# Optimization experiments

Hardware: AMD Instinct MI355X
Metric: run time of the kernel (lower is better)

## Reference

```python
import jax, jax.numpy as jnp
import numpy as np

# dimensions
N = 50000    # nodes
E = 600000   # edges
NS = 64      # scalar (0e) channels of node features
NV = 32      # vector (1o) channels of node features
A = 16       # node attr channels (16x0e)
R = 8        # edge embedding dim (radial basis, 8x0e)
H = 8        # fc_hidden_size
AVG_NB = 12.0  # avg_num_neighbors
# gate layout: NS scalars (silu) + NV gate scalars (sigmoid) gating NV vectors
GS = NS + NV  # 96 scalar channels before gate
NW = NS + NS + NV + NV  # 192 per-edge TP weights (paths: s*Y0->0e, s*Y1->1o, v*Y0->1o, v.Y1->0e)


def setup_inputs() -> dict:
    key = jax.random.key(0)
    ks = jax.random.split(key, 20)
    d = {
        'node_s': jax.random.normal(ks[0], (N, NS), jnp.float32),
        'node_v': jax.random.normal(ks[1], (N, NV, 3), jnp.float32),
        'node_attrs': jax.random.normal(ks[2], (N, A), jnp.float32),
        'edge_emb': jax.random.uniform(ks[3], (E, R), jnp.float32),
        'edge_sh0': jnp.ones((E, 1), jnp.float32),
        'edge_sh1': jax.random.normal(ks[4], (E, 3), jnp.float32),
        'edge_index': jax.random.randint(ks[5], (2, E), 0, N),
        # linear_1 on node feats (per-irrep channel mixing)
        'W1s': jax.random.normal(ks[6], (NS, NS), jnp.float32),
        'W1v': jax.random.normal(ks[7], (NV, NV), jnp.float32),
        # radial MLP producing per-edge TP weights
        'Wm1': jax.random.normal(ks[8], (R, H), jnp.float32),
        'Wm2': jax.random.normal(ks[9], (H, NW), jnp.float32),
        # linear_2: TP out (96x0e+96x1o) -> pre-gate (96x0e+32x1o)
        'W2s': jax.random.normal(ks[10], (GS, GS), jnp.float32),
        'W2v': jax.random.normal(ks[11], (NS + NV, NV), jnp.float32),
        # update UVU TP internal weights (msg x attrs)
        'Wt0': jax.random.normal(ks[12], (NS, A), jnp.float32),
        'Wt1': jax.random.normal(ks[13], (NV, A), jnp.float32),
        # linear_3
        'W3s': jax.random.normal(ks[14], (NS, GS), jnp.float32),
        'W3v': jax.random.normal(ks[15], (NV, NV), jnp.float32),
        # self connection: FullyConnectedTensorProduct(node_feats, attrs -> pre-gate)
        'Wsc0': jax.random.normal(ks[16], (NS, A, GS), jnp.float32),
        'Wsc1': jax.random.normal(ks[17], (NV, A, NV), jnp.float32),
    }
    return d


def _gate(s_all, v):
    # s_all: [.., GS]; first NS scalars -> silu, last NV -> sigmoid gates for vectors
    scal = jax.nn.silu(s_all[..., :NS])
    gates = jax.nn.sigmoid(s_all[..., NS:])
    return scal, v * gates[..., None]


def reference(node_s, node_v, node_attrs, edge_emb, edge_sh0, edge_sh1, edge_index,
              W1s, W1v, Wm1, Wm2, W2s, W2v, Wt0, Wt1, W3s, W3v, Wsc0, Wsc1):
    src, dst = edge_index[0], edge_index[1]

    # ---- message ----
    s1 = (node_s @ W1s) / jnp.sqrt(jnp.float32(NS))                       # [N,NS]
    v1 = jnp.einsum('nuc,uv->nvc', node_v, W1v) / jnp.sqrt(jnp.float32(NV))
    ss = s1[src]   # [E,NS]
    vv = v1[src]   # [E,NV,3]

    # per-edge TP weights from radial MLP
    w = jax.nn.silu(edge_emb @ Wm1) @ Wm2                                 # [E,NW]
    w0a, w1a, w1b, w0b = jnp.split(w, [NS, 2 * NS, 2 * NS + NV], axis=1)

    # UVU tensor product with SH edge attrs (lmax=1)
    t0a = w0a * ss * edge_sh0                                             # [E,NS] 0e
    t0b = w0b * jnp.einsum('euc,ec->eu', vv, edge_sh1)                    # [E,NV] 0e
    t1a = w1a[:, :, None] * ss[:, :, None] * edge_sh1[:, None, :]         # [E,NS,3] 1o
    t1b = w1b[:, :, None] * vv * edge_sh0[:, :, None]                     # [E,NV,3] 1o
    tp_s = jnp.concatenate([t0a, t0b], axis=1)                            # [E,96]
    tp_v = jnp.concatenate([t1a, t1b], axis=1)                            # [E,96,3]

    m_s = (tp_s @ W2s) / jnp.sqrt(jnp.float32(GS))                        # [E,GS]
    m_v = jnp.einsum('euc,uv->evc', tp_v, W2v) / jnp.sqrt(jnp.float32(NS + NV))  # [E,NV,3]
    msg_s, msg_v = _gate(m_s, m_v)                                        # [E,NS], [E,NV,3]

    # ---- update ----
    agg_s = jax.ops.segment_sum(msg_s, dst, num_segments=N) / jnp.sqrt(jnp.float32(AVG_NB))
    agg_v = jax.ops.segment_sum(msg_v, dst, num_segments=N) / jnp.sqrt(jnp.float32(AVG_NB))

    u0 = jnp.einsum('nu,na,ua->nu', agg_s, node_attrs, Wt0) / jnp.sqrt(jnp.float32(A))
    u1 = jnp.einsum('nuc,na,ua->nuc', agg_v, node_attrs, Wt1) / jnp.sqrt(jnp.float32(A))

    f_s = (u0 @ W3s) / jnp.sqrt(jnp.float32(NS))                          # [N,GS]
    f_v = jnp.einsum('nuc,uv->nvc', u1, W3v) / jnp.sqrt(jnp.float32(NV))  # [N,NV,3]

    # self connection (fully connected TP with scalar attrs)
    sc_s = jnp.einsum('nu,na,uav->nv', node_s, node_attrs, Wsc0) / jnp.sqrt(jnp.float32(NS * A))
    sc_v = jnp.einsum('nuc,na,uaw->nwc', node_v, node_attrs, Wsc1) / jnp.sqrt(jnp.float32(NV * A))
    f_s = f_s + sc_s
    f_v = f_v + sc_v

    out_s, out_v = _gate(f_s, f_v)                                        # [N,NS], [N,NV,3]
    return jnp.concatenate([out_s, out_v.reshape(N, NV * 3)], axis=1)     # [N,160]
```

## Files before the change

kernel.cpp:

```cpp
#include <hip/hip_runtime.h>
#include <math.h>

#define N 50000
#define E 600000
#define EPB 16
#define LDK 104

typedef __attribute__((ext_vector_type(8))) short short8;
typedef __attribute__((ext_vector_type(4))) float float4v;

__device__ __forceinline__ float silu_f(float x) { return x / (1.f + __expf(-x)); }
__device__ __forceinline__ float sigm_f(float x) { return 1.f / (1.f + __expf(-x)); }
__device__ __forceinline__ unsigned short f2bf(float f) {
  unsigned u = __float_as_uint(f);
  u += 0x7fff + ((u >> 16) & 1);
  return (unsigned short)(u >> 16);
}
__device__ __forceinline__ float bf2f(unsigned short u) {
  return __uint_as_float(((unsigned)u) << 16);
}

__global__ void k_hist(const int* __restrict__ eidx, int* __restrict__ counts) {
  int e = blockIdx.x * 256 + threadIdx.x;
  if (e < E) atomicAdd(&counts[eidx[E + e]], 1);
}

__global__ __launch_bounds__(1024)
void k_scan(const int* __restrict__ counts, int* __restrict__ row_ptr) {
  __shared__ int ssum[1024];
  const int t = threadIdx.x;
  const int CH = 49;
  int lo = t * CH, hi = min(lo + CH, N);
  int s = 0;
  for (int i = lo; i < hi; i++) s += counts[i];
  ssum[t] = s;
  __syncthreads();
  for (int off = 1; off < 1024; off <<= 1) {
    int v = (t >= off) ? ssum[t - off] : 0;
    __syncthreads();
    ssum[t] += v;
    __syncthreads();
  }
  int run = (t == 0) ? 0 : ssum[t - 1];
  for (int i = lo; i < hi; i++) { row_ptr[i] = run; run += counts[i]; }
  if (t == 1023) row_ptr[N] = ssum[1023];
}

__global__ void k_scatter(const int* __restrict__ eidx, const int* __restrict__ row_ptr,
                          int* __restrict__ woff, int* __restrict__ perm) {
  int e = blockIdx.x * 256 + threadIdx.x;
  if (e < E) {
    int d = eidx[E + e];
    int p = atomicAdd(&woff[d], 1);
    perm[row_ptr[d] + p] = e;
  }
}

__global__ void k_prep(const float* __restrict__ Wsc0, const float* __restrict__ W3s,
                       const float* __restrict__ Wsc1, const float* __restrict__ W3v,
                       const float* __restrict__ W2s, const float* __restrict__ W2v,
                       unsigned short* __restrict__ BT, unsigned short* __restrict__ B2T,
                       unsigned short* __restrict__ w2sTg, unsigned short* __restrict__ w2vTg) {
  const float isq96 = 0.10206207261596575f;
  int i = blockIdx.x * 256 + threadIdx.x;
  if (i < 96 * 1088) {
    int j = i / 1088, k = i % 1088;
    float v;
    if (k < 1024) v = Wsc0[(size_t)k * 96 + j] * 0.03125f;
    else          v = W3s[(size_t)(k - 1024) * 96 + j] * 0.125f;
    BT[i] = f2bf(v);
  } else if (i < 96 * 1088 + 32 * 576) {
    int i2 = i - 96 * 1088;
    int w = i2 / 576, k = i2 % 576;
    float v = 0.f;
    if (k < 512)      v = Wsc1[(size_t)k * 32 + w] * 0.04419417382415922f;
    else if (k < 544) v = W3v[(size_t)(k - 512) * 32 + w] * 0.17677669529663689f;
    B2T[i2] = f2bf(v);
  } else if (i < 96 * 1088 + 32 * 576 + 96 * 96) {
    int i3 = i - (96 * 1088 + 32 * 576);
    int j = i3 / 96, k = i3 % 96;
    w2sTg[i3] = f2bf(W2s[(size_t)k * 96 + j] * isq96);
  } else {
    int i4 = i - (96 * 1088 + 32 * 576 + 96 * 96);
    if (i4 < 32 * 96) {
      int v = i4 / 96, u = i4 % 96;
      w2vTg[i4] = f2bf(W2v[(size_t)u * 32 + v] * isq96);
    }
  }
}

__global__ __launch_bounds__(256, 4)
void k_lin1(const float* __restrict__ node_s, const float* __restrict__ node_v,
            const float* __restrict__ W1s, const float* __restrict__ W1v,
            float* __restrict__ s1, float* __restrict__ v1) {
  __shared__ float w1s[64 * 64];
  __shared__ float w1v[32 * 32];
  for (int i = threadIdx.x; i < 64 * 64; i += 256) w1s[i] = W1s[i];
  for (int i = threadIdx.x; i < 32 * 32; i += 256) w1v[i] = W1v[i];
  __syncthreads();
  const float is_ns = 0.125f;
  const float is_nv = 0.17677669529663689f;
  int gtid = blockIdx.x * 256 + threadIdx.x;
  int stride = gridDim.x * 256;
  for (int i = gtid; i < N * 160; i += stride) {
    int n = i / 160, ch = i % 160;
    if (ch < 64) {
      const float* row = node_s + n * 64;
      float acc = 0.f;
#pragma unroll
      for (int u = 0; u < 64; u++) acc += row[u] * w1s[u * 64 + ch];
      s1[n * 64 + ch] = acc * is_ns;
    } else {
      int p = ch - 64, v = p / 3, c = p % 3;
      const float* row = node_v + n * 96;
      float acc = 0.f;
#pragma unroll
      for (int u = 0; u < 32; u++) acc += row[u * 3 + c] * w1v[u * 32 + v];
      v1[n * 96 + p] = acc * is_nv;
    }
  }
}

template<int STORE>
__global__ __launch_bounds__(256, 4)
void k_msg(const float* __restrict__ s1, const float* __restrict__ v1,
           const float* __restrict__ emb, const float* __restrict__ sh0g,
           const float* __restrict__ sh1g, const int* __restrict__ eidx,
           const int* __restrict__ perm,
           const float* __restrict__ Wm1, const float* __restrict__ Wm2,
           const unsigned short* __restrict__ w2sTg, const unsigned short* __restrict__ w2vTg,
           float* __restrict__ aggs, float* __restrict__ aggv) {
  __shared__ float wm2s[192 * 9];
  __shared__ float wm1s[64];
  __shared__ unsigned short tps[EPB * LDK];
  __shared__ unsigned short tpv[EPB * 3 * LDK];
  __shared__ float gat[EPB][33];
  __shared__ float msL[EPB][65];
  __shared__ float mvL[EPB][97];
  __shared__ float hb[EPB][8];
  __shared__ float sh1b[EPB][4];
  __shared__ float sh0b[EPB];
  __shared__ int ssrc[EPB];
  __shared__ int sdst[EPB];

  const int t = threadIdx.x;
  const int wave = t >> 6, lane = t & 63;
  const int lm = lane & 15, quad = lane >> 4;
  const int subc = t & 15;

  for (int i = t; i < 192 * 8; i += 256) {
    int h = i / 192, c = i % 192;
    wm2s[c * 9 + h] = Wm2[i];
  }
  if (t < 64) wm1s[t] = Wm1[t];

  short8 b1fr[2][3], b2fr[3];
  {
    const int nt0 = wave;
    const int nt1 = (wave + 4 < 6) ? wave + 4 : wave;
    const int nv2 = wave & 1;
#pragma unroll
    for (int kk = 0; kk < 3; kk++) {
      b1fr[0][kk] = *(const short8*)&w2sTg[(nt0 * 16 + lm) * 96 + kk * 32 + quad * 8];
      b1fr[1][kk] = *(const short8*)&w2sTg[(nt1 * 16 + lm) * 96 + kk * 32 + quad * 8];
      b2fr[kk]    = *(const short8*)&w2vTg[(nv2 * 16 + lm) * 96 + kk * 32 + quad * 8];
    }
  }
  __syncthreads();

  for (int pass = blockIdx.x; pass < E / EPB; pass += gridDim.x) {
    const int ebase = pass * EPB;
    __syncthreads();
    if (t < EPB) {
      const int e = STORE ? perm[ebase + t] : (ebase + t);
      ssrc[t] = eidx[e];
      sdst[t] = eidx[E + e];
      sh0b[t] = sh0g[e];
    } else if (t >= 64 && t < 64 + EPB * 3) {
      int i = t - 64;
      const int el = i / 3, c = i % 3;
      const int e = STORE ? perm[ebase + el] : (ebase + el);
      sh1b[el][c] = sh1g[e * 3 + c];
    } else if (t >= 128) {
      int i = t - 128, el = i >> 3, sub = i & 7;
      const int e = STORE ? perm[ebase + el] : (ebase + el);
      float acc = 0.f;
#pragma unroll
      for (int r = 0; r < 8; r++) acc += emb[e * 8 + r] * wm1s[r * 8 + sub];
      hb[el][sub] = silu_f(acc);
    }
    __syncthreads();
    {
      const int el = t >> 4, sub = subc;
      const int src = ssrc[el];
      const float s0v = sh0b[el];
      const float x0 = sh1b[el][0], x1 = sh1b[el][1], x2 = sh1b[el][2];
      float hr[8];
#pragma unroll
      for (int h = 0; h < 8; h++) hr[h] = hb[el][h];
      const float4v ss = *(const float4v*)&s1[(size_t)src * 64 + sub * 4];
      unsigned short tsv[4], tvv[3][4];
#pragma unroll
      for (int i = 0; i < 4; i++) {
        float w0a = 0.f, w1a = 0.f;
#pragma unroll
        for (int h = 0; h < 8; h++) {
          w0a += hr[h] * wm2s[(sub * 4 + i) * 9 + h];
          w1a += hr[h] * wm2s[(64 + sub * 4 + i) * 9 + h];
        }
        const float ssu = ss[i];
        tsv[i] = f2bf(w0a * ssu * s0v);
        const float base = w1a * ssu;
        tvv[0][i] = f2bf(base * x0);
        tvv[1][i] = f2bf(base * x1);
        tvv[2][i] = f2bf(base * x2);
      }
      *(uint2*)&tps[el * LDK + sub * 4] = *(uint2*)tsv;
#pragma unroll
      for (int c = 0; c < 3; c++)
        *(uint2*)&tpv[(el * 3 + c) * LDK + sub * 4] = *(uint2*)tvv[c];
      const float2* vp = (const float2*)&v1[(size_t)src * 96 + sub * 6];
      const float2 va = vp[0], vb = vp[1], vc = vp[2];
      const float v6[6] = {va.x, va.y, vb.x, vb.y, vc.x, vc.y};
      unsigned short ts2[2], tv2[3][2];
#pragma unroll
      for (int i2 = 0; i2 < 2; i2++) {
        float w1b = 0.f, w0b = 0.f;
#pragma unroll
        for (int h = 0; h < 8; h++) {
          w1b += hr[h] * wm2s[(128 + sub * 2 + i2) * 9 + h];
          w0b += hr[h] * wm2s[(160 + sub * 2 + i2) * 9 + h];
        }
        const float vx = v6[i2 * 3 + 0], vy = v6[i2 * 3 + 1], vz = v6[i2 * 3 + 2];
        ts2[i2] = f2bf(w0b * (vx * x0 + vy * x1 + vz * x2));
        tv2[0][i2] = f2bf(w1b * vx * s0v);
        tv2[1][i2] = f2bf(w1b * vy * s0v);
        tv2[2][i2] = f2bf(w1b * vz * s0v);
      }
      *(unsigned*)&tps[el * LDK + 64 + sub * 2] = *(unsigned*)ts2;
#pragma unroll
      for (int c = 0; c < 3; c++)
        *(unsigned*)&tpv[(el * 3 + c) * LDK + 64 + sub * 2] = *(unsigned*)tv2[c];
    }
    __syncthreads();
    if (STORE) {
      short8 afr[3];
#pragma unroll
      for (int kk = 0; kk < 3; kk++)
        afr[kk] = *(const short8*)&tps[lm * LDK + kk * 32 + quad * 8];
#pragma unroll
      for (int tt = 0; tt < 3; tt++) {
        const int id = wave + tt * 4;
        float4v acc = {0.f, 0.f, 0.f, 0.f};
        if (id < 6) {
          const int t2 = id >> 2;
#pragma unroll
          for (int kk = 0; kk < 3; kk++)
            acc = __builtin_amdgcn_mfma_f32_16x16x32_bf16(afr[kk], b1fr[t2][kk], acc, 0, 0, 0);
          const int j = id * 16 + lm;
#pragma unroll
          for (int reg = 0; reg < 4; reg++) {
            const int e = quad * 4 + reg;
            const float val = acc[reg];
            if (j < 64) msL[e][j] = silu_f(val);
            else        gat[e][j - 64] = sigm_f(val);
          }
        } else {
          const int g2 = id - 6;
          const int mt = g2 >> 1, nt2 = g2 & 1;
#pragma unroll
          for (int kk = 0; kk < 3; kk++) {
            short8 a = *(const short8*)&tpv[(mt * 16 + lm) * LDK + kk * 32 + quad * 8];
            acc = __builtin_amdgcn_mfma_f32_16x16x32_bf16(a, b2fr[kk], acc, 0, 0, 0);
          }
          const int v = nt2 * 16 + lm;
#pragma unroll
          for (int reg = 0; reg < 4; reg++) {
            const int r = mt * 16 + quad * 4 + reg;
            const int e = (r * 171) >> 9, c = r - 3 * e;
            mvL[e][v * 3 + c] = acc[reg];
          }
        }
      }
      __syncthreads();
      if (t < 160) {
        const int col = t - 64;
        const int gv = (col * 171) >> 9;
        float acc = 0.f;
        int cur = sdst[0];
        for (int s2 = 0; s2 < EPB; s2++) {
          const int d = sdst[s2];
          const float val = (t < 64) ? msL[s2][t] : mvL[s2][col] * gat[s2][gv];
          if (d != cur) {
            if (t < 64) atomicAdd(&aggs[(size_t)cur * 64 + t], acc);
            else        atomicAdd(&aggv[(size_t)cur * 96 + col], acc);
            acc = 0.f; cur = d;
          }
          acc += val;
        }
        if (t < 64) atomicAdd(&aggs[(size_t)cur * 64 + t], acc);
        else        atomicAdd(&aggv[(size_t)cur * 96 + col], acc);
      }
    } else {
      {
        short8 afr[3];
#pragma unroll
        for (int kk = 0; kk < 3; kk++)
          afr[kk] = *(const short8*)&tps[lm * LDK + kk * 32 + quad * 8];
#pragma unroll
        for (int t2 = 0; t2 < 2; t2++) {
          const int nt = wave + t2 * 4;
          if (nt < 6) {
            float4v acc = {0.f, 0.f, 0.f, 0.f};
#pragma unroll
            for (int kk = 0; kk < 3; kk++)
              acc = __builtin_amdgcn_mfma_f32_16x16x32_bf16(afr[kk], b1fr[t2][kk], acc, 0, 0, 0);
            const int j = nt * 16 + lm;
#pragma unroll
            for (int reg = 0; reg < 4; reg++) {
              const int e = quad * 4 + reg;
              const float val = acc[reg];
              if (j < 64) atomicAdd(&aggs[(size_t)sdst[e] * 64 + j], silu_f(val));
              else        gat[e][j - 64] = sigm_f(val);
            }
          }
        }
      }
      __syncthreads();
#pragma unroll
      for (int t2 = 0; t2 < 2; t2++) {
        const int tile = wave + t2 * 4;
        if (tile < 6) {
          const int mt = tile >> 1, nt2 = tile & 1;
          float4v acc = {0.f, 0.f, 0.f, 0.f};
#pragma unroll
          for (int kk = 0; kk < 3; kk++) {
            short8 a = *(const short8*)&tpv[(mt * 16 + lm) * LDK + kk * 32 + quad * 8];
            acc = __builtin_amdgcn_mfma_f32_16x16x32_bf16(a, b2fr[kk], acc, 0, 0, 0);
          }
          const int v = nt2 * 16 + lm;
#pragma unroll
          for (int reg = 0; reg < 4; reg++) {
            const int r = mt * 16 + quad * 4 + reg;
            const int e = (r * 171) >> 9, c = r - 3 * e;
            atomicAdd(&aggv[(size_t)sdst[e] * 96 + v * 3 + c], acc[reg] * gat[e][v]);
          }
        }
      }
    }
  }
}

__global__ __launch_bounds__(256, 4)
void k_c1(const float* __restrict__ node_s, const float* __restrict__ attrs,
          const float* __restrict__ aggs, const float* __restrict__ Wt0,
          const unsigned short* __restrict__ BT,
          float* __restrict__ out, float* __restrict__ gates) {
  __shared__ float s_row[32][65];
  __shared__ float attr[32][16];
  __shared__ float t0[32][65];
  __shared__ float wt0[1024];
  const int t = threadIdx.x;
  const int wave = t >> 6, lane = t & 63, lm = lane & 15, quad = lane >> 4;
  const int nbase = blockIdx.x * 32;

  for (int i = t; i < 1024; i += 256) wt0[i] = Wt0[i];
  for (int i = t; i < 2048; i += 256) {
    int nl = i >> 6, u = i & 63, n = nbase + nl;
    s_row[nl][u] = (n < N) ? node_s[(size_t)n * 64 + u] : 0.f;
    t0[nl][u]    = (n < N) ? aggs[(size_t)n * 64 + u] : 0.f;
  }
  for (int i = t; i < 512; i += 256) {
    int nl = i >> 4, a = i & 15, n = nbase + nl;
    attr[nl][a] = (n < N) ? attrs[(size_t)n * 16 + a] : 0.f;
  }
  __syncthreads();
  for (int i = t; i < 2048; i += 256) {
    int nl = i >> 6, u = i & 63;
    float d0 = 0.f;
#pragma unroll
    for (int a = 0; a < 16; a++) d0 += attr[nl][a] * wt0[u * 16 + a];
    t0[nl][u] *= d0 * 0.07216878364870322f;
  }
  __syncthreads();

  const int a0 = (quad & 1) * 8;
  float aA0[8], aA1[8];
#pragma unroll
  for (int i = 0; i < 8; i++) {
    aA0[i] = attr[lm][a0 + i];
    aA1[i] = attr[16 + lm][a0 + i];
  }

  float4v acc[3] = {{0,0,0,0},{0,0,0,0},{0,0,0,0}};
  int mts[3], nts[3];
#pragma unroll
  for (int tt = 0; tt < 3; tt++) {
    const int tile = wave + tt * 4;
    mts[tt] = tile / 6;
    nts[tt] = tile % 6;
  }

  for (int kc = 0; kc < 17; kc++) {
#pragma unroll
    for (int ks = 0; ks < 2; ks++) {
      unsigned short e0[8], e1[8];
      if (kc < 16) {
        const int u = kc * 4 + ks * 2 + (quad >> 1);
        const float s0v = s_row[lm][u];
        const float s1v = s_row[16 + lm][u];
#pragma unroll
        for (int i = 0; i < 8; i++) {
          e0[i] = f2bf(s0v * aA0[i]);
          e1[i] = f2bf(s1v * aA1[i]);
        }
      } else {
        const int c0 = ks * 32 + quad * 8;
#pragma unroll
        for (int i = 0; i < 8; i++) {
          e0[i] = f2bf(t0[lm][c0 + i]);
          e1[i] = f2bf(t0[16 + lm][c0 + i]);
        }
      }
      const short8 am0 = *(const short8*)e0;
      const short8 am1 = *(const short8*)e1;
#pragma unroll
      for (int tt = 0; tt < 3; tt++) {
        short8 b = *(const short8*)&BT[(size_t)(nts[tt] * 16 + lm) * 1088 + kc * 64 + ks * 32 + quad * 8];
        acc[tt] = __builtin_amdgcn_mfma_f32_16x16x32_bf16(mts[tt] ? am1 : am0, b, acc[tt], 0, 0, 0);
      }
    }
  }
#pragma unroll
  for (int tt = 0; tt < 3; tt++) {
    const int j = nts[tt] * 16 + lm;
#pragma unroll
    for (int reg = 0; reg < 4; reg++) {
      const int m = mts[tt] * 16 + quad * 4 + reg;
      const int n = nbase + m;
      if (n < N) {
        const float val = acc[tt][reg];
        if (j < 64) out[(size_t)n * 160 + j] = silu_f(val);
        else        gates[(size_t)n * 32 + (j - 64)] = sigm_f(val);
      }
    }
  }
}

__global__ __launch_bounds__(256, 4)
void k_c2(const float* __restrict__ node_v, const float* __restrict__ attrs,
          const float* __restrict__ aggv, const float* __restrict__ Wt1,
          const unsigned short* __restrict__ B2T, const float* __restrict__ gts,
          float* __restrict__ out) {
  __shared__ float nvs[32][97];
  __shared__ float t1s[32][97];
  __shared__ float attr[32][16];
  __shared__ float wt1[512];
  const int t = threadIdx.x;
  const int wave = t >> 6, lane = t & 63, lm = lane & 15, quad = lane >> 4;
  const int nbase = blockIdx.x * 32;

  for (int i = t; i < 512; i += 256) wt1[i] = Wt1[i];
  for (int i = t; i < 32 * 96; i += 256) {
    int nl = i / 96, rr = i % 96, n = nbase + nl;
    nvs[nl][rr] = (n < N) ? node_v[(size_t)n * 96 + rr] : 0.f;
    t1s[nl][rr] = (n < N) ? aggv[(size_t)n * 96 + rr] : 0.f;
  }
  for (int i = t; i < 512; i += 256) {
    int nl = i >> 4, a = i & 15, n = nbase + nl;
    attr[nl][a] = (n < N) ? attrs[(size_t)n * 16 + a] : 0.f;
  }
  __syncthreads();
  for (int i = t; i < 1024; i += 256) {
    int nl = i >> 5, u = i & 31;
    float d1 = 0.f;
#pragma unroll
    for (int a = 0; a < 16; a++) d1 += attr[nl][a] * wt1[u * 16 + a];
    d1 *= 0.07216878364870322f;
    t1s[nl][u * 3 + 0] *= d1; t1s[nl][u * 3 + 1] *= d1; t1s[nl][u * 3 + 2] *= d1;
  }
  __syncthreads();

  int nls[3], cs[3], nts[3], mts[3];
#pragma unroll
  for (int tt = 0; tt < 3; tt++) {
    const int tile = wave + tt * 4;
    mts[tt] = tile >> 1;
    nts[tt] = tile & 1;
    const int row = mts[tt] * 16 + lm;
    nls[tt] = (row * 171) >> 9;
    cs[tt]  = row - 3 * nls[tt];
  }
  const int a0 = (quad & 1) * 8;
  float aA[3][8];
#pragma unroll
  for (int tt = 0; tt < 3; tt++)
#pragma unroll
    for (int i = 0; i < 8; i++) aA[tt][i] = attr[nls[tt]][a0 + i];

  float4v acc[3] = {{0,0,0,0},{0,0,0,0},{0,0,0,0}};

  for (int kc = 0; kc < 9; kc++) {
#pragma unroll
    for (int ks = 0; ks < 2; ks++) {
      if (kc == 8 && ks == 1) continue;
#pragma unroll
      for (int tt = 0; tt < 3; tt++) {
        unsigned short ev[8];
        if (kc < 8) {
          const int u = kc * 4 + ks * 2 + (quad >> 1);
          const float vv = nvs[nls[tt]][u * 3 + cs[tt]];
#pragma unroll
          for (int i = 0; i < 8; i++) ev[i] = f2bf(vv * aA[tt][i]);
        } else {
#pragma unroll
          for (int i = 0; i < 8; i++) ev[i] = f2bf(t1s[nls[tt]][(quad * 8 + i) * 3 + cs[tt]]);
        }
        const short8 a = *(const short8*)ev;
        short8 b = *(const short8*)&B2T[(size_t)(nts[tt] * 16 + lm) * 576 + kc * 64 + ks * 32 + quad * 8];
        acc[tt] = __builtin_amdgcn_mfma_f32_16x16x32_bf16(a, b, acc[tt], 0, 0, 0);
      }
    }
  }
#pragma unroll
  for (int tt = 0; tt < 3; tt++) {
    const int w = nts[tt] * 16 + lm;
#pragma unroll
    for (int reg = 0; reg < 4; reg++) {
      const int row = mts[tt] * 16 + quad * 4 + reg;
      const int nl = (row * 171) >> 9, c = row - 3 * nl;
      const int n = nbase + nl;
      if (n < N)
        out[(size_t)n * 160 + 64 + w * 3 + c] = acc[tt][reg] * gts[(size_t)n * 32 + w];
    }
  }
}

extern "C" void kernel_launch(void* const* d_in, const int* in_sizes, int n_in,
                              void* d_out, int out_size, void* d_ws, size_t ws_size,
                              hipStream_t stream) {
  const float* node_s = (const float*)d_in[0];
  const float* node_v = (const float*)d_in[1];
  const float* attrs  = (const float*)d_in[2];
  const float* emb    = (const float*)d_in[3];
  const float* sh0    = (const float*)d_in[4];
  const float* sh1    = (const float*)d_in[5];
  const int*   eidx   = (const int*)d_in[6];
  const float* W1s    = (const float*)d_in[7];
  const float* W1v    = (const float*)d_in[8];
  const float* Wm1    = (const float*)d_in[9];
  const float* Wm2    = (const float*)d_in[10];
  const float* W2s    = (const float*)d_in[11];
  const float* W2v    = (const float*)d_in[12];
  const float* Wt0    = (const float*)d_in[13];
  const float* Wt1    = (const float*)d_in[14];
  const float* W3s    = (const float*)d_in[15];
  const float* W3v    = (const float*)d_in[16];
  const float* Wsc0   = (const float*)d_in[17];
  const float* Wsc1   = (const float*)d_in[18];

  char* p = (char*)d_ws;
  float* s1  = (float*)p;  p += (size_t)N * 64 * 4;
  float* v1f = (float*)p;  p += (size_t)N * 96 * 4;
  float* gts = (float*)p;  p += (size_t)N * 32 * 4;
  unsigned short* BT    = (unsigned short*)p;  p += (size_t)96 * 1088 * 2;
  unsigned short* B2T   = (unsigned short*)p;  p += (size_t)32 * 576 * 2;
  unsigned short* w2sTg = (unsigned short*)p;  p += (size_t)96 * 96 * 2;
  unsigned short* w2vTg = (unsigned short*)p;  p += (size_t)32 * 96 * 2;
  char* pmode = p;
  size_t base = (size_t)(pmode - (char*)d_ws);
  size_t need_store = base + ((size_t)N + 1) * 4 + (size_t)N * 4 + (size_t)N * 4
                    + (size_t)E * 4 + (size_t)N * 160 * 4;
  const bool store = (ws_size >= need_store);

  k_prep<<<528, 256, 0, stream>>>(Wsc0, W3s, Wsc1, W3v, W2s, W2v, BT, B2T, w2sTg, w2vTg);
  k_lin1<<<1024, 256, 0, stream>>>(node_s, node_v, W1s, W1v, s1, v1f);

  if (store) {
    int* rowp = (int*)pmode;
    int* cnt  = rowp + (N + 1);
    int* woff = cnt + N;
    int* perm = woff + N;
    float* aggs = (float*)(perm + E);
    float* aggv = aggs + (size_t)N * 64;
    hipMemsetAsync(cnt, 0, (size_t)N * 2 * 4, stream);
    hipMemsetAsync(aggs, 0, (size_t)N * 160 * 4, stream);
    k_hist<<<(E + 255) / 256, 256, 0, stream>>>(eidx, cnt);
    k_scan<<<1, 1024, 0, stream>>>(cnt, rowp);
    k_scatter<<<(E + 255) / 256, 256, 0, stream>>>(eidx, rowp, woff, perm);
    k_msg<1><<<1024, 256, 0, stream>>>(s1, v1f, emb, sh0, sh1, eidx, perm, Wm1, Wm2,
                                       w2sTg, w2vTg, aggs, aggv);
    k_c1<<<1563, 256, 0, stream>>>(node_s, attrs, aggs, Wt0, BT, (float*)d_out, gts);
    k_c2<<<1563, 256, 0, stream>>>(node_v, attrs, aggv, Wt1, B2T, gts, (float*)d_out);
  } else {
    float* aggs = (float*)pmode;
    float* aggv = aggs + (size_t)N * 64;
    hipMemsetAsync(aggs, 0, (size_t)N * 160 * 4, stream);
    k_msg<0><<<1024, 256, 0, stream>>>(s1, v1f, emb, sh0, sh1, eidx, nullptr, Wm1, Wm2,
                                       w2sTg, w2vTg, aggs, aggv);
    k_c1<<<1563, 256, 0, stream>>>(node_s, attrs, aggs, Wt0, BT, (float*)d_out, gts);
    k_c2<<<1563, 256, 0, stream>>>(node_v, attrs, aggv, Wt1, B2T, gts, (float*)d_out);
  }
}
```

Baseline: 696.1 us.

## Merge prep, lin1 and memsets into one init kernel; bf16 message staging

Combines the weight-prep kernel, the linear_1 kernel and the two memsets into a single k_init launch that splits its work by block range. This is meant to cut launch and serialization overhead between small stages. Separately, the per-edge message staging buffers in shared memory move from fp32 to bf16, which lowers LDS use. k_msg now targets 5 blocks per CU with a grid of 1280 blocks. The bf16 staging loses precision in the aggregated messages, and the tighter launch bound may cause register spills.

```diff
diff --git a/kernel.cpp b/kernel.cpp
--- a/kernel.cpp
+++ b/kernel.cpp
@@ -1,5 +1,6 @@
 #include <hip/hip_runtime.h>
 #include <math.h>
+#include <stdint.h>
 
 #define N 50000
 #define E 600000
@@ -56,73 +57,87 @@
   }
 }
 
-__global__ void k_prep(const float* __restrict__ Wsc0, const float* __restrict__ W3s,
-                       const float* __restrict__ Wsc1, const float* __restrict__ W3v,
-                       const float* __restrict__ W2s, const float* __restrict__ W2v,
-                       unsigned short* __restrict__ BT, unsigned short* __restrict__ B2T,
-                       unsigned short* __restrict__ w2sTg, unsigned short* __restrict__ w2vTg) {
-  const float isq96 = 0.10206207261596575f;
-  int i = blockIdx.x * 256 + threadIdx.x;
-  if (i < 96 * 1088) {
-    int j = i / 1088, k = i % 1088;
-    float v;
-    if (k < 1024) v = Wsc0[(size_t)k * 96 + j] * 0.03125f;
-    else          v = W3s[(size_t)(k - 1024) * 96 + j] * 0.125f;
-    BT[i] = f2bf(v);
-  } else if (i < 96 * 1088 + 32 * 576) {
-    int i2 = i - 96 * 1088;
-    int w = i2 / 576, k = i2 % 576;
-    float v = 0.f;
-    if (k < 512)      v = Wsc1[(size_t)k * 32 + w] * 0.04419417382415922f;
-    else if (k < 544) v = W3v[(size_t)(k - 512) * 32 + w] * 0.17677669529663689f;
-    B2T[i2] = f2bf(v);
-  } else if (i < 96 * 1088 + 32 * 576 + 96 * 96) {
-    int i3 = i - (96 * 1088 + 32 * 576);
-    int j = i3 / 96, k = i3 % 96;
-    w2sTg[i3] = f2bf(W2s[(size_t)k * 96 + j] * isq96);
-  } else {
-    int i4 = i - (96 * 1088 + 32 * 576 + 96 * 96);
-    if (i4 < 32 * 96) {
-      int v = i4 / 96, u = i4 % 96;
-      w2vTg[i4] = f2bf(W2v[(size_t)u * 32 + v] * isq96);
-    }
-  }
-}
-
-__global__ __launch_bounds__(256, 4)
-void k_lin1(const float* __restrict__ node_s, const float* __restrict__ node_v,
+__global__ __launch_bounds__(256)
+void k_init(const float* __restrict__ Wsc0, const float* __restrict__ W3s,
+            const float* __restrict__ Wsc1, const float* __restrict__ W3v,
+            const float* __restrict__ W2s, const float* __restrict__ W2v,
+            unsigned short* __restrict__ BT, unsigned short* __restrict__ B2T,
+            unsigned short* __restrict__ w2sTg, unsigned short* __restrict__ w2vTg,
+            const float* __restrict__ node_s, const float* __restrict__ node_v,
             const float* __restrict__ W1s, const float* __restrict__ W1v,
-            float* __restrict__ s1, float* __restrict__ v1) {
+            float* __restrict__ s1, float* __restrict__ v1,
+            int* __restrict__ cnt, float* __restrict__ aggs) {
   __shared__ float w1s[64 * 64];
   __shared__ float w1v[32 * 32];
-  for (int i = threadIdx.x; i < 64 * 64; i += 256) w1s[i] = W1s[i];
-  for (int i = threadIdx.x; i < 32 * 32; i += 256) w1v[i] = W1v[i];
-  __syncthreads();
-  const float is_ns = 0.125f;
-  const float is_nv = 0.17677669529663689f;
-  int gtid = blockIdx.x * 256 + threadIdx.x;
-  int stride = gridDim.x * 256;
-  for (int i = gtid; i < N * 160; i += stride) {
-    int n = i / 160, ch = i % 160;
-    if (ch < 64) {
-      const float* row = node_s + n * 64;
-      float acc = 0.f;
-#pragma unroll
-      for (int u = 0; u < 64; u++) acc += row[u] * w1s[u * 64 + ch];
-      s1[n * 64 + ch] = acc * is_ns;
+  const int b = blockIdx.x, t = threadIdx.x;
+  const float isq96 = 0.10206207261596575f;
+
+  if (b < 528) {
+    int i = b * 256 + t;
+    if (i < 96 * 1088) {
+      int j = i / 1088, k = i % 1088;
+      float v;
+      if (k < 1024) v = Wsc0[(size_t)k * 96 + j] * 0.03125f;
+      else          v = W3s[(size_t)(k - 1024) * 96 + j] * 0.125f;
+      BT[i] = f2bf(v);
+    } else if (i < 96 * 1088 + 32 * 576) {
+      int i2 = i - 96 * 1088;
+      int w = i2 / 576, k = i2 % 576;
+      float v = 0.f;
+      if (k < 512)      v = Wsc1[(size_t)k * 32 + w] * 0.04419417382415922f;
+      else if (k < 544) v = W3v[(size_t)(k - 512) * 32 + w] * 0.17677669529663689f;
+      B2T[i2] = f2bf(v);
+    } else if (i < 96 * 1088 + 32 * 576 + 96 * 96) {
+      int i3 = i - (96 * 1088 + 32 * 576);
+      int j = i3 / 96, k = i3 % 96;
+      w2sTg[i3] = f2bf(W2s[(size_t)k * 96 + j] * isq96);
     } else {
-      int p = ch - 64, v = p / 3, c = p % 3;
-      const float* row = node_v + n * 96;
-      float acc = 0.f;
-#pragma unroll
-      for (int u = 0; u < 32; u++) acc += row[u * 3 + c] * w1v[u * 32 + v];
-      v1[n * 96 + p] = acc * is_nv;
-    }
+      int i4 = i - (96 * 1088 + 32 * 576 + 96 * 96);
+      if (i4 < 32 * 96) {
+        int v = i4 / 96, u = i4 % 96;
+        w2vTg[i4] = f2bf(W2v[(size_t)u * 32 + v] * isq96);
+      }
+    }
+  } else if (b < 1552) {
+    for (int i = t; i < 64 * 64; i += 256) w1s[i] = W1s[i];
+    for (int i = t; i < 32 * 32; i += 256) w1v[i] = W1v[i];
+    __syncthreads();
+    const float is_ns = 0.125f;
+    const float is_nv = 0.17677669529663689f;
+    int gtid = (b - 528) * 256 + t;
+    const int stride = 1024 * 256;
+    for (int i = gtid; i < N * 160; i += stride) {
+      int n = i / 160, ch = i % 160;
+      if (ch < 64) {
+        const float* row = node_s + n * 64;
+        float acc = 0.f;
+#pragma unroll
+        for (int u = 0; u < 64; u++) acc += row[u] * w1s[u * 64 + ch];
+        s1[n * 64 + ch] = acc * is_ns;
+      } else {
+        int p = ch - 64, v = p / 3, c = p % 3;
+        const float* row = node_v + n * 96;
+        float acc = 0.f;
+#pragma unroll
+        for (int u = 0; u < 32; u++) acc += row[u * 3 + c] * w1v[u * 32 + v];
+        v1[n * 96 + p] = acc * is_nv;
+      }
+    }
+  } else if (b < 1943) {
+    if (cnt) {
+      int idx = (b - 1552) * 256 + t;
+      if (idx < 2 * N) cnt[idx] = 0;
+    }
+  } else {
+    float4v* a4 = (float4v*)aggs;
+    const int tot = N * 160 / 4;
+    const float4v z = {0.f, 0.f, 0.f, 0.f};
+    for (int i = (b - 1943) * 256 + t; i < tot; i += 2000 * 256) a4[i] = z;
   }
 }
 
 template<int STORE>
-__global__ __launch_bounds__(256, 4)
+__global__ __launch_bounds__(256, 5)
 void k_msg(const float* __restrict__ s1, const float* __restrict__ v1,
            const float* __restrict__ emb, const float* __restrict__ sh0g,
            const float* __restrict__ sh1g, const int* __restrict__ eidx,
@@ -135,8 +150,8 @@
   __shared__ unsigned short tps[EPB * LDK];
   __shared__ unsigned short tpv[EPB * 3 * LDK];
   __shared__ float gat[EPB][33];
-  __shared__ float msL[EPB][65];
-  __shared__ float mvL[EPB][97];
+  __shared__ unsigned short msL[EPB][66];
+  __shared__ unsigned short mvL[EPB][98];
   __shared__ float hb[EPB][8];
   __shared__ float sh1b[EPB][4];
   __shared__ float sh0b[EPB];
@@ -262,7 +277,7 @@
           for (int reg = 0; reg < 4; reg++) {
             const int e = quad * 4 + reg;
             const float val = acc[reg];
-            if (j < 64) msL[e][j] = silu_f(val);
+            if (j < 64) msL[e][j] = f2bf(silu_f(val));
             else        gat[e][j - 64] = sigm_f(val);
           }
         } else {
@@ -278,7 +293,7 @@
           for (int reg = 0; reg < 4; reg++) {
             const int r = mt * 16 + quad * 4 + reg;
             const int e = (r * 171) >> 9, c = r - 3 * e;
-            mvL[e][v * 3 + c] = acc[reg];
+            mvL[e][v * 3 + c] = f2bf(acc[reg]);
           }
         }
       }
@@ -290,7 +305,8 @@
         int cur = sdst[0];
         for (int s2 = 0; s2 < EPB; s2++) {
           const int d = sdst[s2];
-          const float val = (t < 64) ? msL[s2][t] : mvL[s2][col] * gat[s2][gv];
+          const float val = (t < 64) ? bf2f(msL[s2][t])
+                                     : bf2f(mvL[s2][col]) * gat[s2][gv];
           if (d != cur) {
             if (t < 64) atomicAdd(&aggs[(size_t)cur * 64 + t], acc);
             else        atomicAdd(&aggv[(size_t)cur * 96 + col], acc);
@@ -570,33 +586,31 @@
   char* pmode = p;
   size_t base = (size_t)(pmode - (char*)d_ws);
   size_t need_store = base + ((size_t)N + 1) * 4 + (size_t)N * 4 + (size_t)N * 4
-                    + (size_t)E * 4 + (size_t)N * 160 * 4;
+                    + (size_t)E * 4 + 16 + (size_t)N * 160 * 4;
   const bool store = (ws_size >= need_store);
-
-  k_prep<<<528, 256, 0, stream>>>(Wsc0, W3s, Wsc1, W3v, W2s, W2v, BT, B2T, w2sTg, w2vTg);
-  k_lin1<<<1024, 256, 0, stream>>>(node_s, node_v, W1s, W1v, s1, v1f);
 
   if (store) {
     int* rowp = (int*)pmode;
     int* cnt  = rowp + (N + 1);
     int* woff = cnt + N;
     int* perm = woff + N;
-    float* aggs = (float*)(perm + E);
+    float* aggs = (float*)(((uintptr_t)(perm + E) + 15) & ~(uintptr_t)15);
     float* aggv = aggs + (size_t)N * 64;
-    hipMemsetAsync(cnt, 0, (size_t)N * 2 * 4, stream);
-    hipMemsetAsync(aggs, 0, (size_t)N * 160 * 4, stream);
+    k_init<<<3943, 256, 0, stream>>>(Wsc0, W3s, Wsc1, W3v, W2s, W2v, BT, B2T, w2sTg, w2vTg,
+                                     node_s, node_v, W1s, W1v, s1, v1f, cnt, aggs);
     k_hist<<<(E + 255) / 256, 256, 0, stream>>>(eidx, cnt);
     k_scan<<<1, 1024, 0, stream>>>(cnt, rowp);
     k_scatter<<<(E + 255) / 256, 256, 0, stream>>>(eidx, rowp, woff, perm);
-    k_msg<1><<<1024, 256, 0, stream>>>(s1, v1f, emb, sh0, sh1, eidx, perm, Wm1, Wm2,
+    k_msg<1><<<1280, 256, 0, stream>>>(s1, v1f, emb, sh0, sh1, eidx, perm, Wm1, Wm2,
                                        w2sTg, w2vTg, aggs, aggv);
     k_c1<<<1563, 256, 0, stream>>>(node_s, attrs, aggs, Wt0, BT, (float*)d_out, gts);
     k_c2<<<1563, 256, 0, stream>>>(node_v, attrs, aggv, Wt1, B2T, gts, (float*)d_out);
   } else {
     float* aggs = (float*)pmode;
     float* aggv = aggs + (size_t)N * 64;
-    hipMemsetAsync(aggs, 0, (size_t)N * 160 * 4, stream);
-    k_msg<0><<<1024, 256, 0, stream>>>(s1, v1f, emb, sh0, sh1, eidx, nullptr, Wm1, Wm2,
+    k_init<<<3943, 256, 0, stream>>>(Wsc0, W3s, Wsc1, W3v, W2s, W2v, BT, B2T, w2sTg, w2vTg,
+                                     node_s, node_v, W1s, W1v, s1, v1f, nullptr, aggs);
+    k_msg<0><<<1280, 256, 0, stream>>>(s1, v1f, emb, sh0, sh1, eidx, nullptr, Wm1, Wm2,
                                        w2sTg, w2vTg, aggs, aggv);
     k_c1<<<1563, 256, 0, stream>>>(node_s, attrs, aggs, Wt0, BT, (float*)d_out, gts);
     k_c2<<<1563, 256, 0, stream>>>(node_v, attrs, aggv, Wt1, B2T, gts, (float*)d_out);
```

Result: slower. 722.3 us (+3.8%).
